# Performance work log

Hardware: AMD Instinct MI355X
Metric: run time of the kernel (lower is better)

The kernel has to match this reference:

```python
import jax, jax.numpy as jnp
import numpy as np

N_EMBD = 1024
N_HEAD = 16
HEAD_DIM = N_EMBD // N_HEAD


def setup_inputs() -> dict:
    key = jax.random.key(0)
    k1, k2, k3, k4, k5 = jax.random.split(key, 5)
    B, T = 2, 2048
    x = jax.random.normal(k1, (B, T, N_EMBD), dtype=jnp.float32)
    # c_attn: Dense(3*n_embd), c_proj: Dense(n_embd); flax Dense kernel is [in, out]
    s = 0.02
    W_attn = jax.random.normal(k2, (N_EMBD, 3 * N_EMBD), dtype=jnp.float32) * s
    b_attn = jnp.zeros((3 * N_EMBD,), dtype=jnp.float32)
    W_proj = jax.random.normal(k3, (N_EMBD, N_EMBD), dtype=jnp.float32) * s
    b_proj = jnp.zeros((N_EMBD,), dtype=jnp.float32)
    return {"x": x, "W_attn": W_attn, "b_attn": b_attn, "W_proj": W_proj, "b_proj": b_proj}


def reference(x, W_attn, b_attn, W_proj, b_proj):
    B, T, C = x.shape
    qkv = x @ W_attn + b_attn                      # [B,T,3C]
    q, k, v = jnp.split(qkv, 3, axis=-1)
    q = q.reshape(B, T, N_HEAD, HEAD_DIM).transpose(0, 2, 1, 3)  # [B,H,T,D]
    k = k.reshape(B, T, N_HEAD, HEAD_DIM).transpose(0, 2, 1, 3)
    v = v.reshape(B, T, N_HEAD, HEAD_DIM).transpose(0, 2, 1, 3)
    scale = 1.0 / jnp.sqrt(jnp.float32(HEAD_DIM))
    att = jnp.einsum('bhqd,bhkd->bhqk', q, k) * scale            # [B,H,T,T]
    causal = jnp.tril(jnp.ones((T, T), dtype=bool))
    att = jnp.where(causal, att, -jnp.inf)
    att = jax.nn.softmax(att, axis=-1)
    y = jnp.einsum('bhqk,bhkd->bhqd', att, v)                    # [B,H,T,D]
    y = y.transpose(0, 2, 1, 3).reshape(B, T, C)
    return y @ W_proj + b_proj
```

## Files before the change

kernel.cpp:

```cpp
#include <hip/hip_runtime.h>
#include <hip/hip_bf16.h>
#include <math.h>

#define N_EMBD 1024
#define N_HEAD 16
#define HEAD_DIM 64
#define BSZ 2
#define TSEQ 2048
#define C3 (3 * N_EMBD)

typedef __attribute__((ext_vector_type(8))) short short8_t;
typedef __attribute__((ext_vector_type(4))) float f32x4;
typedef __attribute__((address_space(3))) unsigned int lds_u32;
typedef const __attribute__((address_space(1))) unsigned int glb_u32;

__device__ __forceinline__ unsigned short f2bf(float f) {
  return __builtin_bit_cast(unsigned short, __float2bfloat16(f));
}

__global__ __launch_bounds__(256) void conv_vec(
    const float* __restrict__ in, unsigned short* __restrict__ out, int n8)
{
  for (int i = blockIdx.x * blockDim.x + threadIdx.x; i < n8;
       i += gridDim.x * blockDim.x) {
    float4 a = ((const float4*)in)[2 * i];
    float4 b = ((const float4*)in)[2 * i + 1];
    union { unsigned short u[8]; uint4 q; } t;
    t.u[0] = f2bf(a.x); t.u[1] = f2bf(a.y); t.u[2] = f2bf(a.z); t.u[3] = f2bf(a.w);
    t.u[4] = f2bf(b.x); t.u[5] = f2bf(b.y); t.u[6] = f2bf(b.z); t.u[7] = f2bf(b.w);
    ((uint4*)out)[i] = t.q;
  }
}

__global__ __launch_bounds__(256) void conv_transpose(
    const float* __restrict__ in, unsigned short* __restrict__ out, int K, int N)
{
  __shared__ float tile[32][33];
  const int bk = blockIdx.y * 32, bn = blockIdx.x * 32;
  const int r = threadIdx.x >> 3, c4 = (threadIdx.x & 7) * 4;
  *(float4*)&tile[r][c4] = *(const float4*)(in + (size_t)(bk + r) * N + bn + c4);
  __syncthreads();
  union { unsigned short u[4]; uint2 q; } t;
#pragma unroll
  for (int j = 0; j < 4; ++j) t.u[j] = f2bf(tile[c4 + j][r]);
  *(uint2*)(out + (size_t)(bn + r) * K + bk + c4) = t.q;
}

template <typename OUT_T>
__global__ __launch_bounds__(256) void gemm_mfma(
    const unsigned short* __restrict__ A,
    const unsigned short* __restrict__ Bt,
    const float* __restrict__ bias,
    OUT_T* __restrict__ C, int M, int N, int K)
{
  constexpr int BM = 128, BN = 128, BK = 32;
  __shared__ __align__(16) unsigned short As[BM * BK];
  __shared__ __align__(16) unsigned short Bs[BN * BK];

  const int tid = threadIdx.x;
  const int l = tid & 63;
  const int g = l >> 4, c = l & 15;
  const int w = tid >> 6;
  const int wr = w >> 1, wc = w & 1;
  const int bm = blockIdx.y * BM, bn = blockIdx.x * BN;

  f32x4 acc[4][4];
#pragma unroll
  for (int i = 0; i < 4; i++)
#pragma unroll
    for (int j = 0; j < 4; j++) acc[i][j] = (f32x4){0.f, 0.f, 0.f, 0.f};

  int srow[2], skq[2];
#pragma unroll
  for (int i = 0; i < 2; i++) {
    int seg = i * 256 + tid;
    srow[i] = seg >> 2;
    skq[i] = (seg & 3) ^ (srow[i] & 3);
  }

  for (int k0 = 0; k0 < K; k0 += BK) {
    __syncthreads();
#pragma unroll
    for (int i = 0; i < 2; i++) {
      int seg = i * 256 + tid;
      __builtin_amdgcn_global_load_lds(
          (glb_u32*)(A + (size_t)(bm + srow[i]) * K + k0 + skq[i] * 8),
          (lds_u32*)((char*)As + seg * 16), 16, 0, 0);
      __builtin_amdgcn_global_load_lds(
          (glb_u32*)(Bt + (size_t)(bn + srow[i]) * K + k0 + skq[i] * 8),
          (lds_u32*)((char*)Bs + seg * 16), 16, 0, 0);
    }
    __syncthreads();

    short8_t af[4], bf[4];
#pragma unroll
    for (int mi = 0; mi < 4; mi++) {
      int row = wr * 64 + mi * 16 + c;
      af[mi] = *(const short8_t*)((char*)As + row * 64 + ((g * 16) ^ ((row & 3) << 4)));
    }
#pragma unroll
    for (int ni = 0; ni < 4; ni++) {
      int row = wc * 64 + ni * 16 + c;
      bf[ni] = *(const short8_t*)((char*)Bs + row * 64 + ((g * 16) ^ ((row & 3) << 4)));
    }
    __builtin_amdgcn_s_setprio(1);
#pragma unroll
    for (int mi = 0; mi < 4; mi++)
#pragma unroll
      for (int ni = 0; ni < 4; ni++)
        acc[mi][ni] = __builtin_amdgcn_mfma_f32_16x16x32_bf16(af[mi], bf[ni], acc[mi][ni], 0, 0, 0);
    __builtin_amdgcn_s_setprio(0);
  }

  float bv[4];
#pragma unroll
  for (int ni = 0; ni < 4; ni++) bv[ni] = bias[bn + wc * 64 + ni * 16 + c];
#pragma unroll
  for (int mi = 0; mi < 4; mi++)
#pragma unroll
    for (int j = 0; j < 4; j++) {
      int row = bm + wr * 64 + mi * 16 + g * 4 + j;
      OUT_T* cp = C + (size_t)row * N + bn + wc * 64 + c;
#pragma unroll
      for (int ni = 0; ni < 4; ni++) {
        float v = acc[mi][ni][j] + bv[ni];
        if constexpr (sizeof(OUT_T) == 2)
          *(unsigned short*)(cp + ni * 16) = f2bf(v);
        else
          *(float*)(cp + ni * 16) = v;
      }
    }
}

__global__ __launch_bounds__(256) void attn_mfma(
    const unsigned short* __restrict__ qkv, unsigned short* __restrict__ y)
{
  const int l = threadIdx.x & 63;
  const int w = threadIdx.x >> 6;
  const int b = blockIdx.z, h = blockIdx.y;
  const int pair = blockIdx.x;
  const int g = l >> 4;
  const int c = l & 15;

  __shared__ __align__(16) unsigned short Ks[64 * 64];
  __shared__ __align__(16) unsigned short Vt[64 * 64];
  __shared__ __align__(16) unsigned short Ps[4][16 * 64];

  const unsigned short* base = qkv + (size_t)b * TSEQ * C3;

#pragma unroll 1
  for (int half = 0; half < 2; ++half) {
    const int tile = half == 0 ? (31 - pair) : pair;
    const int r0 = tile * 64;
    const int qr0 = r0 + w * 16;

    short8_t qf[2];
    {
      const unsigned short* qp = base + (size_t)(qr0 + c) * C3 + h * HEAD_DIM + g * 8;
      qf[0] = *(const short8_t*)(qp);
      qf[1] = *(const short8_t*)(qp + 32);
    }

    f32x4 o[4];
    float m[4], ld[4];
#pragma unroll
    for (int dt = 0; dt < 4; ++dt) o[dt] = (f32x4){0.f, 0.f, 0.f, 0.f};
#pragma unroll
    for (int r = 0; r < 4; ++r) { m[r] = -1e30f; ld[r] = 0.f; }

    const int nch = tile + 1;
#pragma unroll 1
    for (int ci = 0; ci < nch; ++ci) {
      const int k0 = ci * 64;
      __syncthreads();
#pragma unroll
      for (int s = 0; s < 2; ++s) {
        int seg = threadIdx.x + s * 256;
        int kr = seg >> 3, d8 = (seg & 7) * 8;
        uint4 t = *(const uint4*)(base + (size_t)(k0 + kr) * C3 + N_EMBD + h * HEAD_DIM + d8);
        *(uint4*)((char*)Ks + kr * 128 + ((d8 * 2) ^ ((kr & 7) << 4))) = t;
      }
      {
        int dd = threadIdx.x & 63, kq = (threadIdx.x >> 6) * 16;
        const unsigned short* vp = base + (size_t)(k0 + kq) * C3 + 2 * N_EMBD + h * HEAD_DIM + dd;
        union { unsigned short u[16]; uint4 q[2]; } t;
#pragma unroll
        for (int j = 0; j < 16; ++j) t.u[j] = vp[(size_t)j * C3];
        char* vrow = (char*)Vt + dd * 128;
        *(uint4*)(vrow + ((kq * 2) ^ ((dd & 7) << 4)))      = t.q[0];
        *(uint4*)(vrow + ((kq * 2 + 16) ^ ((dd & 7) << 4))) = t.q[1];
      }
      __syncthreads();
      if (k0 > qr0 + 15) continue;

      f32x4 st[4];
      __builtin_amdgcn_s_setprio(1);
#pragma unroll
      for (int kt = 0; kt < 4; ++kt) {
        const int row = kt * 16 + c;
        short8_t kf0 = *(const short8_t*)((const char*)Ks + row * 128 + ((g * 16) ^ ((row & 7) << 4)));
        short8_t kf1 = *(const short8_t*)((const char*)Ks + row * 128 + ((64 + g * 16) ^ ((row & 7) << 4)));
        f32x4 a2 = (f32x4){0.f, 0.f, 0.f, 0.f};
        a2 = __builtin_amdgcn_mfma_f32_16x16x32_bf16(qf[0], kf0, a2, 0, 0, 0);
        a2 = __builtin_amdgcn_mfma_f32_16x16x32_bf16(qf[1], kf1, a2, 0, 0, 0);
        st[kt] = a2;
      }
      __builtin_amdgcn_s_setprio(0);
#pragma unroll
      for (int r = 0; r < 4; ++r) {
        const int qg = qr0 + g * 4 + r;
        float mx = -1e30f;
#pragma unroll
        for (int kt = 0; kt < 4; ++kt) {
          int kg = k0 + kt * 16 + c;
          float s = (kg <= qg) ? st[kt][r] * 0.125f : -1e30f;
          st[kt][r] = s;
          mx = fmaxf(mx, s);
        }
        mx = fmaxf(mx, __shfl_xor(mx, 1));
        mx = fmaxf(mx, __shfl_xor(mx, 2));
        mx = fmaxf(mx, __shfl_xor(mx, 4));
        mx = fmaxf(mx, __shfl_xor(mx, 8));
        float mnew = fmaxf(m[r], mx);
        float corr = __expf(m[r] - mnew);
        m[r] = mnew;
        float rs = 0.f;
        const int row = g * 4 + r;
#pragma unroll
        for (int kt = 0; kt < 4; ++kt) {
          int kg = k0 + kt * 16 + c;
          float p = (kg <= qg) ? __expf(st[kt][r] - mnew) : 0.f;
          rs += p;
          *(unsigned short*)((char*)Ps[w] + row * 128 +
                             (((kt * 16 + c) * 2) ^ ((row & 7) << 4))) = f2bf(p);
        }
        rs += __shfl_xor(rs, 1);
        rs += __shfl_xor(rs, 2);
        rs += __shfl_xor(rs, 4);
        rs += __shfl_xor(rs, 8);
        ld[r] = ld[r] * corr + rs;
#pragma unroll
        for (int dt = 0; dt < 4; ++dt) o[dt][r] *= corr;
      }
      short8_t pf[2];
#pragma unroll
      for (int kc = 0; kc < 2; ++kc)
        pf[kc] = *(const short8_t*)((const char*)Ps[w] + c * 128 +
                                    ((64 * kc + g * 16) ^ ((c & 7) << 4)));
      __builtin_amdgcn_s_setprio(1);
#pragma unroll
      for (int dt = 0; dt < 4; ++dt) {
        const int row = dt * 16 + c;
#pragma unroll
        for (int kc = 0; kc < 2; ++kc) {
          short8_t vf = *(const short8_t*)((const char*)Vt + row * 128 +
                                           ((64 * kc + g * 16) ^ ((row & 7) << 4)));
          o[dt] = __builtin_amdgcn_mfma_f32_16x16x32_bf16(pf[kc], vf, o[dt], 0, 0, 0);
        }
      }
      __builtin_amdgcn_s_setprio(0);
    }
#pragma unroll
    for (int r = 0; r < 4; ++r) {
      float inv = 1.f / ld[r];
      const size_t rowoff = ((size_t)b * TSEQ + qr0 + g * 4 + r) * N_EMBD + h * HEAD_DIM;
#pragma unroll
      for (int dt = 0; dt < 4; ++dt)
        y[rowoff + dt * 16 + c] = f2bf(o[dt][r] * inv);
    }
  }
}

extern "C" void kernel_launch(void* const* d_in, const int* in_sizes, int n_in,
                              void* d_out, int out_size, void* d_ws, size_t ws_size,
                              hipStream_t stream) {
  const float* x      = (const float*)d_in[0];
  const float* W_attn = (const float*)d_in[1];
  const float* b_attn = (const float*)d_in[2];
  const float* W_proj = (const float*)d_in[3];
  const float* b_proj = (const float*)d_in[4];
  float* out = (float*)d_out;

  const int M = BSZ * TSEQ;

  unsigned short* xb   = (unsigned short*)d_ws;
  unsigned short* Wta  = xb + (size_t)M * N_EMBD;
  unsigned short* Wtp  = Wta + (size_t)C3 * N_EMBD;
  unsigned short* qkvb = Wtp + (size_t)N_EMBD * N_EMBD;
  unsigned short* yatt = qkvb + (size_t)M * C3;

  conv_vec<<<2048, 256, 0, stream>>>(x, xb, M * N_EMBD / 8);
  conv_transpose<<<dim3(C3 / 32, N_EMBD / 32), 256, 0, stream>>>(W_attn, Wta, N_EMBD, C3);
  conv_transpose<<<dim3(N_EMBD / 32, N_EMBD / 32), 256, 0, stream>>>(W_proj, Wtp, N_EMBD, N_EMBD);

  gemm_mfma<unsigned short><<<dim3(C3 / 128, M / 128), 256, 0, stream>>>(
      xb, Wta, b_attn, qkvb, M, C3, N_EMBD);

  attn_mfma<<<dim3(TSEQ / 128, N_HEAD, BSZ), 256, 0, stream>>>(qkvb, yatt);

  gemm_mfma<float><<<dim3(N_EMBD / 128, M / 128), 256, 0, stream>>>(
      yatt, Wtp, b_proj, out, M, N_EMBD, N_EMBD);
}
```

Baseline: 227.2 us.

## Pre-transpose V into a per-head layout and use exp2 softmax with masking only on diagonal tiles

Adds a kernel that transposes V from the fused QKV buffer into a [b,h,d,t] layout. This lets the attention kernel load V tiles with 16-byte vector loads instead of 16 strided scalar loads per thread. The softmax now folds log2(e) into the scale and uses exp2f, and applies the causal mask only on chunks that cross the diagonal. The cost is an extra kernel launch plus an extra round trip of V through global memory.

Result: slower. 233.3 us (+2.7%).

```diff
diff --git a/kernel.cpp b/kernel.cpp
--- a/kernel.cpp
+++ b/kernel.cpp
@@ -46,6 +46,25 @@
   *(uint2*)(out + (size_t)(bn + r) * K + bk + c4) = t.q;
 }
 
+__global__ __launch_bounds__(256) void conv_vT(
+    const unsigned short* __restrict__ qkv, unsigned short* __restrict__ vt)
+{
+  __shared__ unsigned short tile[32][36];
+  const int t0 = blockIdx.x * 32;
+  const int d0 = blockIdx.y * 32;
+  const int bh = blockIdx.z;
+  const int b = bh >> 4, h = bh & 15;
+  const int r = threadIdx.x >> 3, c4 = (threadIdx.x & 7) * 4;
+  const unsigned short* src =
+      qkv + ((size_t)b * TSEQ + t0 + r) * C3 + 2 * N_EMBD + h * HEAD_DIM + d0 + c4;
+  *(uint2*)&tile[r][c4] = *(const uint2*)src;
+  __syncthreads();
+  union { unsigned short u[4]; uint2 q; } o;
+#pragma unroll
+  for (int j = 0; j < 4; ++j) o.u[j] = tile[c4 + j][r];
+  *(uint2*)(vt + ((size_t)bh * HEAD_DIM + d0 + r) * TSEQ + t0 + c4) = o.q;
+}
+
 template <typename OUT_T>
 __global__ __launch_bounds__(256) void gemm_mfma(
     const unsigned short* __restrict__ A,
@@ -133,7 +152,9 @@
 }
 
 __global__ __launch_bounds__(256) void attn_mfma(
-    const unsigned short* __restrict__ qkv, unsigned short* __restrict__ y)
+    const unsigned short* __restrict__ qkv,
+    const unsigned short* __restrict__ vt,
+    unsigned short* __restrict__ y)
 {
   const int l = threadIdx.x & 63;
   const int w = threadIdx.x >> 6;
@@ -147,6 +168,8 @@
   __shared__ __align__(16) unsigned short Ps[4][16 * 64];
 
   const unsigned short* base = qkv + (size_t)b * TSEQ * C3;
+  const unsigned short* vbase = vt + (size_t)(b * N_HEAD + h) * HEAD_DIM * TSEQ;
+  const float SCALE_LOG2E = 0.125f * 1.44269504f;
 
 #pragma unroll 1
   for (int half = 0; half < 2; ++half) {
@@ -180,15 +203,12 @@
         uint4 t = *(const uint4*)(base + (size_t)(k0 + kr) * C3 + N_EMBD + h * HEAD_DIM + d8);
         *(uint4*)((char*)Ks + kr * 128 + ((d8 * 2) ^ ((kr & 7) << 4))) = t;
       }
-      {
-        int dd = threadIdx.x & 63, kq = (threadIdx.x >> 6) * 16;
-        const unsigned short* vp = base + (size_t)(k0 + kq) * C3 + 2 * N_EMBD + h * HEAD_DIM + dd;
-        union { unsigned short u[16]; uint4 q[2]; } t;
-#pragma unroll
-        for (int j = 0; j < 16; ++j) t.u[j] = vp[(size_t)j * C3];
-        char* vrow = (char*)Vt + dd * 128;
-        *(uint4*)(vrow + ((kq * 2) ^ ((dd & 7) << 4)))      = t.q[0];
-        *(uint4*)(vrow + ((kq * 2 + 16) ^ ((dd & 7) << 4))) = t.q[1];
+#pragma unroll
+      for (int s = 0; s < 2; ++s) {
+        int seg = threadIdx.x + s * 256;
+        int dr = seg >> 3, k8 = (seg & 7) * 8;
+        uint4 t = *(const uint4*)(vbase + (size_t)dr * TSEQ + k0 + k8);
+        *(uint4*)((char*)Vt + dr * 128 + ((k8 * 2) ^ ((dr & 7) << 4))) = t;
       }
       __syncthreads();
       if (k0 > qr0 + 15) continue;
@@ -206,14 +226,16 @@
         st[kt] = a2;
       }
       __builtin_amdgcn_s_setprio(0);
+
+      const bool full = (k0 + 63 <= qr0);
 #pragma unroll
       for (int r = 0; r < 4; ++r) {
         const int qg = qr0 + g * 4 + r;
         float mx = -1e30f;
 #pragma unroll
         for (int kt = 0; kt < 4; ++kt) {
-          int kg = k0 + kt * 16 + c;
-          float s = (kg <= qg) ? st[kt][r] * 0.125f : -1e30f;
+          float s = st[kt][r] * SCALE_LOG2E;
+          if (!full) { int kg = k0 + kt * 16 + c; if (kg > qg) s = -1e30f; }
           st[kt][r] = s;
           mx = fmaxf(mx, s);
         }
@@ -222,14 +244,13 @@
         mx = fmaxf(mx, __shfl_xor(mx, 4));
         mx = fmaxf(mx, __shfl_xor(mx, 8));
         float mnew = fmaxf(m[r], mx);
-        float corr = __expf(m[r] - mnew);
+        float corr = exp2f(m[r] - mnew);
         m[r] = mnew;
         float rs = 0.f;
         const int row = g * 4 + r;
 #pragma unroll
         for (int kt = 0; kt < 4; ++kt) {
-          int kg = k0 + kt * 16 + c;
-          float p = (kg <= qg) ? __expf(st[kt][r] - mnew) : 0.f;
+          float p = exp2f(st[kt][r] - mnew);
           rs += p;
           *(unsigned short*)((char*)Ps[w] + row * 128 +
                              (((kt * 16 + c) * 2) ^ ((row & 7) << 4))) = f2bf(p);
@@ -288,6 +309,7 @@
   unsigned short* Wtp  = Wta + (size_t)C3 * N_EMBD;
   unsigned short* qkvb = Wtp + (size_t)N_EMBD * N_EMBD;
   unsigned short* yatt = qkvb + (size_t)M * C3;
+  unsigned short* vtb  = yatt + (size_t)M * N_EMBD;
 
   conv_vec<<<2048, 256, 0, stream>>>(x, xb, M * N_EMBD / 8);
   conv_transpose<<<dim3(C3 / 32, N_EMBD / 32), 256, 0, stream>>>(W_attn, Wta, N_EMBD, C3);
@@ -296,7 +318,9 @@
   gemm_mfma<unsigned short><<<dim3(C3 / 128, M / 128), 256, 0, stream>>>(
       xb, Wta, b_attn, qkvb, M, C3, N_EMBD);
 
-  attn_mfma<<<dim3(TSEQ / 128, N_HEAD, BSZ), 256, 0, stream>>>(qkvb, yatt);
+  conv_vT<<<dim3(TSEQ / 32, HEAD_DIM / 32, BSZ * N_HEAD), 256, 0, stream>>>(qkvb, vtb);
+
+  attn_mfma<<<dim3(TSEQ / 128, N_HEAD, BSZ), 256, 0, stream>>>(qkvb, vtb, yatt);
 
   gemm_mfma<float><<<dim3(N_EMBD / 128, M / 128), 256, 0, stream>>>(
       yatt, Wtp, b_proj, out, M, N_EMBD, N_EMBD);
```
